# Performance work log

Measured on AMD Instinct MI355X. Metric: run time of the kernel, lower is better.

Reference implementation:

```python
import jax, jax.numpy as jnp
import numpy as np

# Static config (Phi-3-medium style)
HIDDEN = 5120
N_HEADS = 40
N_KV_HEADS = 10
HEAD_DIM = 128  # padded == original here
ROPE_THETA = 10000.0
B, S = 8, 1024  # 8 packed sequences of length 1024 -> T = 8192
T = B * S


def apply_rope(x, pos, theta=ROPE_THETA):
    # x: [T, N, H], pos: [T]  (neox-style split-half rotary over full head dim)
    H = x.shape[-1]
    half = H // 2
    inv_freq = 1.0 / (theta ** (jnp.arange(half, dtype=jnp.float32) * 2.0 / H))
    ang = pos.astype(jnp.float32)[:, None] * inv_freq  # [T, half]
    cos = jnp.cos(ang)[:, None, :]  # [T, 1, half]
    sin = jnp.sin(ang)[:, None, :]
    x1, x2 = x[..., :half], x[..., half:]
    return jnp.concatenate([x1 * cos - x2 * sin, x2 * cos + x1 * sin], axis=-1).astype(x.dtype)


def setup_inputs() -> dict:
    key = jax.random.key(0)
    k1, k2, k3 = jax.random.split(key, 3)
    x = jax.random.normal(k1, (T, HIDDEN), dtype=jnp.float32)
    w_qkv = jax.random.normal(k2, (HIDDEN, N_HEADS + 2 * N_KV_HEADS, HEAD_DIM), dtype=jnp.float32) * (HIDDEN ** -0.5)
    w_o = jax.random.normal(k3, (N_HEADS, HEAD_DIM, HIDDEN), dtype=jnp.float32) * ((N_HEADS * HEAD_DIM) ** -0.5)
    positions = jnp.tile(jnp.arange(S, dtype=jnp.int32), B)  # per-sequence positions
    return {"x": x, "w_qkv": w_qkv, "w_o": w_o, "positions": positions}


def reference(x, w_qkv, w_o, positions):
    # Fused QKV projection: [T, D] x [D, N_total, H] -> [T, N_total, H]
    qkv = jnp.einsum('td,dnh->tnh', x, w_qkv)
    q, k, v = jnp.split(qkv, [N_HEADS, N_HEADS + N_KV_HEADS], axis=1)
    q = apply_rope(q, positions)
    k = apply_rope(k, positions)

    # KV cache is simply the (rope'd) k/v written at token slots (no quantization).
    G = N_HEADS // N_KV_HEADS  # GQA group size
    qb = q.reshape(B, S, N_KV_HEADS, G, HEAD_DIM)
    kb = k.reshape(B, S, N_KV_HEADS, HEAD_DIM)
    vb = v.reshape(B, S, N_KV_HEADS, HEAD_DIM)

    scale = HEAD_DIM ** -0.5
    scores = jnp.einsum('bqkgh,bskh->bkgqs', qb, kb) * scale  # [B,K,G,S,S]
    causal = jnp.tril(jnp.ones((S, S), dtype=bool))
    scores = jnp.where(causal, scores, jnp.finfo(scores.dtype).min)
    probs = jax.nn.softmax(scores, axis=-1)
    out = jnp.einsum('bkgqs,bskh->bqkgh', probs, vb)  # [B,S,K,G,H]
    out = out.reshape(T, N_HEADS, HEAD_DIM)

    o = jnp.einsum('tnh,nhd->td', out, w_o)
    return o
```

## Files before the change

### kernel.cpp

```cpp
#include <hip/hip_runtime.h>
#include <hip/hip_bf16.h>

typedef unsigned short u16;
typedef __attribute__((ext_vector_type(8))) __bf16 bf16x8;
typedef __attribute__((ext_vector_type(4))) float f32x4;

#define GLDS16(gsrc, ldst)                                                         \
  __builtin_amdgcn_global_load_lds(                                               \
      (__attribute__((address_space(1))) const void*)(gsrc),                      \
      (__attribute__((address_space(3))) void*)(ldst), 16, 0, 0)

__device__ __forceinline__ float bf2f(u16 u) {
  union { unsigned int i; float f; } v; v.i = ((unsigned int)u) << 16; return v.f;
}
__device__ __forceinline__ u16 f2bf(float f) {
  union { float f; unsigned int i; } v; v.f = f;
  return (u16)((v.i + 0x7fffu + ((v.i >> 16) & 1u)) >> 16);
}

__global__ void cvt_x_kernel(const float4* __restrict__ in, ushort4* __restrict__ out) {
  size_t i = (size_t)blockIdx.x * 256 + threadIdx.x;
  float4 v = in[i];
  ushort4 o;
  o.x = f2bf(v.x); o.y = f2bf(v.y); o.z = f2bf(v.z); o.w = f2bf(v.w);
  out[i] = o;
}

__global__ void tconv_kernel(const float* __restrict__ in, u16* __restrict__ out,
                             int R, int C) {
  __shared__ float tile[64][65];
  const int c0 = blockIdx.x * 64, r0 = blockIdx.y * 64;
  const int tx = threadIdx.x & 63, ty = threadIdx.x >> 6;
#pragma unroll
  for (int p = 0; p < 16; ++p) {
    int row = p * 4 + ty;
    tile[row][tx] = in[(size_t)(r0 + row) * C + c0 + tx];
  }
  __syncthreads();
#pragma unroll
  for (int p = 0; p < 16; ++p) {
    int row = p * 4 + ty;
    out[(size_t)(c0 + row) * R + r0 + tx] = f2bf(tile[tx][row]);
  }
}

__global__ __launch_bounds__(256, 2) void gemm_bt_kernel(
    const u16* __restrict__ A, const u16* __restrict__ BT,
    float* __restrict__ Cf, u16* __restrict__ Cb, int M, int N, int K,
    int nbx, int nby) {
  const int PW = 8;
  const int per_panel = nby * PW;
  const int bid = blockIdx.x;
  const int panel = bid / per_panel;
  const int rem = bid - panel * per_panel;
  const int pw = min(PW, nbx - panel * PW);
  const int bn = panel * PW + rem % pw;
  const int bm = rem / pw;

  __shared__ __align__(16) u16 As[128 * 32];
  __shared__ __align__(16) u16 Bs[128 * 32];
  const int tid = threadIdx.x;
  const int wave = tid >> 6, lane = tid & 63;
  const int quad = lane >> 4, l16 = lane & 15;
  const int m0 = bm * 128, n0 = bn * 128;
  const int wm = (wave >> 1) * 64, wn = (wave & 1) * 64;
  const int rck = lane >> 2;
  const int kc = (lane & 3) * 8;

  f32x4 acc[4][4] = {};

  const size_t a0 = (size_t)(m0 + 16 * wave + rck) * K;
  const size_t a1 = (size_t)(m0 + 16 * (wave + 4) + rck) * K;
  const size_t b0 = (size_t)(n0 + 16 * wave + rck) * K;
  const size_t b1 = (size_t)(n0 + 16 * (wave + 4) + rck) * K;

  for (int k0 = 0; k0 < K; k0 += 32) {
    __syncthreads();
    GLDS16(A + a0 + k0 + kc, As + 512 * wave);
    GLDS16(A + a1 + k0 + kc, As + 512 * (wave + 4));
    GLDS16(BT + b0 + k0 + kc, Bs + 512 * wave);
    GLDS16(BT + b1 + k0 + kc, Bs + 512 * (wave + 4));
    __syncthreads();
    bf16x8 af[4], bfr[4];
#pragma unroll
    for (int t = 0; t < 4; ++t)
      af[t] = *(const bf16x8*)(As + (wm + 16 * t + l16) * 32 + quad * 8);
#pragma unroll
    for (int t = 0; t < 4; ++t)
      bfr[t] = *(const bf16x8*)(Bs + (wn + 16 * t + l16) * 32 + quad * 8);
#pragma unroll
    for (int mt = 0; mt < 4; ++mt)
#pragma unroll
      for (int nt = 0; nt < 4; ++nt)
        acc[mt][nt] = __builtin_amdgcn_mfma_f32_16x16x32_bf16(af[mt], bfr[nt], acc[mt][nt], 0, 0, 0);
  }
#pragma unroll
  for (int mt = 0; mt < 4; ++mt)
#pragma unroll
    for (int nt = 0; nt < 4; ++nt)
#pragma unroll
      for (int r = 0; r < 4; ++r) {
        int row = m0 + wm + 16 * mt + quad * 4 + r;
        int col = n0 + wn + 16 * nt + l16;
        float v = acc[mt][nt][r];
        if (Cb) Cb[(size_t)row * N + col] = f2bf(v);
        else    Cf[(size_t)row * N + col] = v;
      }
}

__global__ void rope_kernel(u16* __restrict__ qkv, const int* __restrict__ positions) {
  int idx = blockIdx.x * 256 + threadIdx.x;
  int j = idx & 63, t = idx >> 6;
  float inv = exp2f(-(float)j * 0.20762050593046014f);
  float ang = (float)positions[t] * inv;
  float sn, cs;
  sincosf(ang, &sn, &cs);
  u16* row = qkv + (size_t)t * 7680;
#pragma unroll 2
  for (int h = 0; h < 50; ++h) {
    u16* p1 = row + h * 128 + j;
    float x1 = bf2f(p1[0]), x2 = bf2f(p1[64]);
    p1[0] = f2bf(x1 * cs - x2 * sn);
    p1[64] = f2bf(x2 * cs + x1 * sn);
  }
}

__global__ void vtrans_kernel(const u16* __restrict__ qkv, u16* __restrict__ vt) {
  __shared__ u16 tile[64][132];
  const int s0 = blockIdx.x * 64, kvh = blockIdx.y, b = blockIdx.z;
  const int tid = threadIdx.x;
#pragma unroll
  for (int p = 0; p < 8; ++p) {
    int sl = p * 8 + (tid >> 5);
    int d = (tid & 31) * 4;
    const u16* src = qkv + (size_t)(b * 1024 + s0 + sl) * 7680 + (50 + kvh) * 128 + d;
    ushort4 v = *(const ushort4*)src;
    tile[sl][d] = v.x; tile[sl][d + 1] = v.y; tile[sl][d + 2] = v.z; tile[sl][d + 3] = v.w;
  }
  __syncthreads();
#pragma unroll
  for (int p = 0; p < 8; ++p) {
    int d = p * 16 + (tid >> 4);
    int sl = (tid & 15) * 4;
    ushort4 v;
    v.x = tile[sl][d]; v.y = tile[sl + 1][d]; v.z = tile[sl + 2][d]; v.w = tile[sl + 3][d];
    u16* dst = vt + ((size_t)((b * 10 + kvh) * 128) + d) * 1024 + s0 + sl;
    *(ushort4*)dst = v;
  }
}

__global__ __launch_bounds__(256, 2) void attn_kernel(
    const u16* __restrict__ qkv, const u16* __restrict__ vt, u16* __restrict__ ao) {
  __shared__ __align__(16) u16 Ks[4][2048];
  __shared__ __align__(16) u16 VTs[2][4096];
  __shared__ __align__(16) u16 Ps[4][2][1024];

  const int tid = threadIdx.x, wave = tid >> 6, lane = tid & 63;
  const int quad = lane >> 4, l16 = lane & 15;
  const int q0 = blockIdx.x * 128, h = blockIdx.y, b = blockIdx.z;
  const int kvh = h >> 2;
  const float SCALE = 0.08838834764831845f;

  bf16x8 qf[2][4];
#pragma unroll
  for (int mt = 0; mt < 2; ++mt) {
    int t = b * 1024 + q0 + wave * 32 + mt * 16 + l16;
    const u16* qrow = qkv + (size_t)t * 7680 + h * 128;
#pragma unroll
    for (int ks = 0; ks < 4; ++ks)
      qf[mt][ks] = *(const bf16x8*)(qrow + ks * 32 + quad * 8);
  }

  f32x4 oa[2][8] = {};
  float mstate[2][4], lstate[2][4];
#pragma unroll
  for (int mt = 0; mt < 2; ++mt)
#pragma unroll
    for (int r = 0; r < 4; ++r) { mstate[mt][r] = -1e30f; lstate[mt][r] = 0.f; }

  const u16* Kbase = qkv + (size_t)(b * 1024) * 7680 + (40 + kvh) * 128;
  const u16* VTbase = vt + (size_t)((b * 10 + kvh) * 128) * 1024;

  const int nsteps = q0 / 64 + 2;
  for (int step = 0; step < nsteps; ++step) {
    const int s0 = step * 64;
    __syncthreads();
#pragma unroll
    for (int j = 0; j < 4; ++j) {
      int c = 4 * wave + j;
      int ksub = c >> 2, rg = c & 3;
      GLDS16(Kbase + (size_t)(s0 + rg * 16 + (lane >> 2)) * 7680 + ksub * 32 + (lane & 3) * 8,
             &Ks[ksub][rg * 512]);
      int vsub = c >> 3, dg = c & 7;
      GLDS16(VTbase + (size_t)(dg * 16 + (lane >> 2)) * 1024 + s0 + vsub * 32 + (lane & 3) * 8,
             &VTs[vsub][dg * 512]);
    }
    __syncthreads();

    f32x4 sa[2][4] = {};
#pragma unroll
    for (int ks = 0; ks < 4; ++ks) {
      bf16x8 kb[4];
#pragma unroll
      for (int nt = 0; nt < 4; ++nt)
        kb[nt] = *(const bf16x8*)&Ks[ks][(nt * 16 + l16) * 32 + quad * 8];
#pragma unroll
      for (int mt = 0; mt < 2; ++mt)
#pragma unroll
        for (int nt = 0; nt < 4; ++nt)
          sa[mt][nt] = __builtin_amdgcn_mfma_f32_16x16x32_bf16(qf[mt][ks], kb[nt], sa[mt][nt], 0, 0, 0);
    }

#pragma unroll
    for (int mt = 0; mt < 2; ++mt) {
#pragma unroll
      for (int r = 0; r < 4; ++r) {
        int qg = q0 + wave * 32 + mt * 16 + quad * 4 + r;
        float pv[4];
        float rowmax = -1e30f;
#pragma unroll
        for (int nt = 0; nt < 4; ++nt) {
          int sg = s0 + nt * 16 + l16;
          float v = sa[mt][nt][r] * SCALE;
          if (sg > qg) v = -1e30f;
          pv[nt] = v;
          rowmax = fmaxf(rowmax, v);
        }
#pragma unroll
        for (int off = 1; off < 16; off <<= 1)
          rowmax = fmaxf(rowmax, __shfl_xor(rowmax, off));
        float mnew = fmaxf(mstate[mt][r], rowmax);
        float alpha = __expf(mstate[mt][r] - mnew);
        mstate[mt][r] = mnew;
        float rs = 0.f;
#pragma unroll
        for (int nt = 0; nt < 4; ++nt) {
          float p = __expf(pv[nt] - mnew);
          rs += p;
          Ps[wave][nt >> 1][(mt * 16 + quad * 4 + r) * 32 + (nt & 1) * 16 + l16] = f2bf(p);
        }
#pragma unroll
        for (int off = 1; off < 16; off <<= 1)
          rs += __shfl_xor(rs, off);
        lstate[mt][r] = lstate[mt][r] * alpha + rs;
#pragma unroll
        for (int ntd = 0; ntd < 8; ++ntd) oa[mt][ntd][r] *= alpha;
      }
    }
    __syncthreads();

#pragma unroll
    for (int ks2 = 0; ks2 < 2; ++ks2) {
      bf16x8 pf[2];
#pragma unroll
      for (int mt = 0; mt < 2; ++mt)
        pf[mt] = *(const bf16x8*)&Ps[wave][ks2][(mt * 16 + l16) * 32 + quad * 8];
#pragma unroll
      for (int ntd = 0; ntd < 8; ++ntd) {
        bf16x8 vf = *(const bf16x8*)&VTs[ks2][(ntd * 16 + l16) * 32 + quad * 8];
#pragma unroll
        for (int mt = 0; mt < 2; ++mt)
          oa[mt][ntd] = __builtin_amdgcn_mfma_f32_16x16x32_bf16(pf[mt], vf, oa[mt][ntd], 0, 0, 0);
      }
    }
  }

#pragma unroll
  for (int mt = 0; mt < 2; ++mt)
#pragma unroll
    for (int ntd = 0; ntd < 8; ++ntd)
#pragma unroll
      for (int r = 0; r < 4; ++r) {
        int t = b * 1024 + q0 + wave * 32 + mt * 16 + quad * 4 + r;
        int d = ntd * 16 + l16;
        float v = oa[mt][ntd][r] / lstate[mt][r];
        ao[((size_t)t * 40 + h) * 128 + d] = f2bf(v);
      }
}

extern "C" void kernel_launch(void* const* d_in, const int* in_sizes, int n_in,
                              void* d_out, int out_size, void* d_ws, size_t ws_size,
                              hipStream_t stream) {
  const float* x = (const float*)d_in[0];
  const float* wqkv = (const float*)d_in[1];
  const float* wo = (const float*)d_in[2];
  const int* pos = (const int*)d_in[3];
  float* out = (float*)d_out;

  char* ws = (char*)d_ws;
  u16* xb = (u16*)(ws);
  u16* wT = (u16*)(ws + 83886080);
  u16* qkvb = (u16*)(ws + 83886080 + 78643200);
  u16* vt = (u16*)(ws + 83886080 + 78643200 + 125829120);

  cvt_x_kernel<<<40960, 256, 0, stream>>>((const float4*)x, (ushort4*)xb);
  tconv_kernel<<<dim3(120, 80), 256, 0, stream>>>(wqkv, wT, 5120, 7680);
  gemm_bt_kernel<<<60 * 64, 256, 0, stream>>>(xb, wT, nullptr, qkvb, 8192, 7680, 5120, 60, 64);
  rope_kernel<<<2048, 256, 0, stream>>>(qkvb, pos);
  vtrans_kernel<<<dim3(16, 10, 8), 256, 0, stream>>>(qkvb, vt);
  tconv_kernel<<<dim3(80, 80), 256, 0, stream>>>(wo, wT, 5120, 5120);
  attn_kernel<<<dim3(8, 40, 8), 256, 0, stream>>>(qkvb, vt, xb);
  gemm_bt_kernel<<<40 * 64, 256, 0, stream>>>(xb, wT, out, nullptr, 8192, 5120, 5120, 40, 64);
}
```

Measured before the change: 2.333 ms.

## Replace 128x128 GEMM with double-buffered 256x256 tile GEMM using swizzled LDS

Both projection GEMMs now use a 512-thread kernel that computes 256x256 output tiles with 128-wide K steps. Global-to-LDS loads are double-buffered and interleaved with MFMA phases under manual waitcnt and barrier control. The LDS layout is XOR-swizzled to avoid bank conflicts, and the workgroup order is remapped for L2 locality. This targets low data reuse and exposed load latency in the old 128x128 single-buffered loop, at the cost of more LDS and registers per block and reduced occupancy.

```diff
diff --git a/kernel.cpp b/kernel.cpp
--- a/kernel.cpp
+++ b/kernel.cpp
@@ -9,6 +9,23 @@
   __builtin_amdgcn_global_load_lds(                                               \
       (__attribute__((address_space(1))) const void*)(gsrc),                      \
       (__attribute__((address_space(3))) void*)(ldst), 16, 0, 0)
+
+#define BAR() asm volatile("s_barrier" ::: "memory")
+#define LG0()                                            \
+  {                                                      \
+    asm volatile("s_waitcnt lgkmcnt(0)" ::: "memory");   \
+    __builtin_amdgcn_sched_barrier(0);                   \
+  }
+#define VMW2()                                           \
+  {                                                      \
+    asm volatile("s_waitcnt vmcnt(2)" ::: "memory");     \
+    __builtin_amdgcn_sched_barrier(0);                   \
+  }
+#define VMW0()                                           \
+  {                                                      \
+    asm volatile("s_waitcnt vmcnt(0)" ::: "memory");     \
+    __builtin_amdgcn_sched_barrier(0);                   \
+  }
 
 __device__ __forceinline__ float bf2f(u16 u) {
   union { unsigned int i; float f; } v; v.i = ((unsigned int)u) << 16; return v.f;
@@ -44,64 +61,157 @@
   }
 }
 
-__global__ __launch_bounds__(256, 2) void gemm_bt_kernel(
+__device__ __forceinline__ void lda4(bf16x8 a[4][2], const u16* b0, const u16* b1) {
+#pragma unroll
+  for (int mt = 0; mt < 4; ++mt) {
+    a[mt][0] = *(const bf16x8*)(b0 + mt * 1024);
+    a[mt][1] = *(const bf16x8*)(b1 + mt * 1024);
+  }
+}
+__device__ __forceinline__ void ldb2(bf16x8 b[2][2], const u16* b0, const u16* b1) {
+#pragma unroll
+  for (int nt = 0; nt < 2; ++nt) {
+    b[nt][0] = *(const bf16x8*)(b0 + nt * 1024);
+    b[nt][1] = *(const bf16x8*)(b1 + nt * 1024);
+  }
+}
+template <int MH, int NH>
+__device__ __forceinline__ void mma8(f32x4 acc[8][4], const bf16x8 a[4][2], const bf16x8 b[2][2]) {
+  __builtin_amdgcn_s_setprio(1);
+#pragma unroll
+  for (int mt = 0; mt < 4; ++mt)
+#pragma unroll
+    for (int nt = 0; nt < 2; ++nt) {
+      f32x4 c = acc[MH * 4 + mt][NH * 2 + nt];
+      c = __builtin_amdgcn_mfma_f32_16x16x32_bf16(a[mt][0], b[nt][0], c, 0, 0, 0);
+      c = __builtin_amdgcn_mfma_f32_16x16x32_bf16(a[mt][1], b[nt][1], c, 0, 0, 0);
+      acc[MH * 4 + mt][NH * 2 + nt] = c;
+    }
+  __builtin_amdgcn_s_setprio(0);
+}
+
+__global__ __launch_bounds__(512, 2) void gemm_bt256_kernel(
     const u16* __restrict__ A, const u16* __restrict__ BT,
     float* __restrict__ Cf, u16* __restrict__ Cb, int M, int N, int K,
-    int nbx, int nby) {
-  const int PW = 8;
-  const int per_panel = nby * PW;
-  const int bid = blockIdx.x;
-  const int panel = bid / per_panel;
-  const int rem = bid - panel * per_panel;
-  const int pw = min(PW, nbx - panel * PW);
+    int nbm, int nbn) {
+  __shared__ __align__(16) u16 As_[2][16384];
+  __shared__ __align__(16) u16 Bs_[2][16384];
+  u16* As0 = &As_[0][0]; u16* As1 = &As_[1][0];
+  u16* Bs0 = &Bs_[0][0]; u16* Bs1 = &Bs_[1][0];
+
+  const int nwg = nbm * nbn;
+  int wg = (int)blockIdx.x;
+  wg = (wg & 7) * (nwg >> 3) + (wg >> 3);
+  const int PW = 10;
+  const int per_panel = PW * nbm;
+  const int panel = wg / per_panel;
+  const int rem = wg - panel * per_panel;
+  const int pw = min(PW, nbn - panel * PW);
   const int bn = panel * PW + rem % pw;
   const int bm = rem / pw;
-
-  __shared__ __align__(16) u16 As[128 * 32];
-  __shared__ __align__(16) u16 Bs[128 * 32];
+  const int m0 = bm * 256, n0 = bn * 256;
+
   const int tid = threadIdx.x;
   const int wave = tid >> 6, lane = tid & 63;
   const int quad = lane >> 4, l16 = lane & 15;
-  const int m0 = bm * 128, n0 = bn * 128;
-  const int wm = (wave >> 1) * 64, wn = (wave & 1) * 64;
-  const int rck = lane >> 2;
-  const int kc = (lane & 3) * 8;
-
-  f32x4 acc[4][4] = {};
-
-  const size_t a0 = (size_t)(m0 + 16 * wave + rck) * K;
-  const size_t a1 = (size_t)(m0 + 16 * (wave + 4) + rck) * K;
-  const size_t b0 = (size_t)(n0 + 16 * wave + rck) * K;
-  const size_t b1 = (size_t)(n0 + 16 * (wave + 4) + rck) * K;
-
-  for (int k0 = 0; k0 < K; k0 += 32) {
-    __syncthreads();
-    GLDS16(A + a0 + k0 + kc, As + 512 * wave);
-    GLDS16(A + a1 + k0 + kc, As + 512 * (wave + 4));
-    GLDS16(BT + b0 + k0 + kc, Bs + 512 * wave);
-    GLDS16(BT + b1 + k0 + kc, Bs + 512 * (wave + 4));
-    __syncthreads();
-    bf16x8 af[4], bfr[4];
-#pragma unroll
-    for (int t = 0; t < 4; ++t)
-      af[t] = *(const bf16x8*)(As + (wm + 16 * t + l16) * 32 + quad * 8);
-#pragma unroll
-    for (int t = 0; t < 4; ++t)
-      bfr[t] = *(const bf16x8*)(Bs + (wn + 16 * t + l16) * 32 + quad * 8);
-#pragma unroll
-    for (int mt = 0; mt < 4; ++mt)
-#pragma unroll
-      for (int nt = 0; nt < 4; ++nt)
-        acc[mt][nt] = __builtin_amdgcn_mfma_f32_16x16x32_bf16(af[mt], bfr[nt], acc[mt][nt], 0, 0, 0);
-  }
-#pragma unroll
-  for (int mt = 0; mt < 4; ++mt)
+  const int wm = wave >> 2, wn = wave & 3;
+
+  const int rl = lane >> 3;
+  const int cs = ((lane & 7) ^ rl) * 8;
+  const u16* pA = A + (size_t)(m0 + wave * 8 + rl) * K + cs;
+  const u16* pB = BT + (size_t)(n0 + wave * 8 + rl) * K + cs;
+  const size_t r64 = (size_t)64 * K, r128 = (size_t)128 * K;
+
+#define STG(p, hofs, kt, lds)                                         \
+  {                                                                   \
+    GLDS16((p) + (hofs) + (size_t)(kt) * 64, (lds) + wave * 512);     \
+    GLDS16((p) + (hofs) + r64 + (size_t)(kt) * 64, (lds) + 4096 + wave * 512); \
+  }
+
+  const int eo = l16 & 7;
+  const int aoff0 = l16 * 64 + ((quad ^ eo) * 8);
+  const int aoff1 = l16 * 64 + (((4 | quad) ^ eo) * 8);
+  const u16* Ab0 = As0 + wm * 8192;
+  const u16* Ab1 = As1 + wm * 8192;
+  const u16* Bb0 = Bs0 + wn * 4096;
+  const u16* Bb1 = Bs1 + wn * 4096;
+
+  f32x4 acc[8][4] = {};
+  bf16x8 a[4][2], b[2][2];
+
+  const int NIT = K >> 7;
+
+  STG(pA, 0, 0, As0);
+  STG(pA, r128, 0, As0 + 8192);
+  STG(pB, 0, 0, Bs0);
+  STG(pB, r128, 0, Bs0 + 8192);
+  STG(pA, 0, 1, As1);
+  VMW2();
+  BAR();
+
+#pragma unroll 1
+  for (int it = 0; it < NIT; ++it) {
+    const int t = 2 * it;
+    const bool sg = (it < NIT - 1);
+
+    lda4(a, Ab0 + aoff0, Ab0 + aoff1);
+    ldb2(b, Bb0 + aoff0, Bb0 + aoff1);
+    STG(pA, r128, t + 1, As1 + 8192);
+    BAR(); LG0();
+    mma8<0, 0>(acc, a, b);
+    BAR();
+    ldb2(b, Bb0 + 2048 + aoff0, Bb0 + 2048 + aoff1);
+    STG(pB, 0, t + 1, Bs1);
+    BAR(); LG0();
+    mma8<0, 1>(acc, a, b);
+    BAR();
+    lda4(a, Ab0 + 4096 + aoff0, Ab0 + 4096 + aoff1);
+    STG(pB, r128, t + 1, Bs1 + 8192);
+    BAR(); LG0();
+    mma8<1, 1>(acc, a, b);
+    BAR();
+    ldb2(b, Bb0 + aoff0, Bb0 + aoff1);
+    if (sg) STG(pA, 0, t + 2, As0);
+    BAR(); LG0();
+    mma8<1, 0>(acc, a, b);
+    if (sg) { VMW2(); } else { VMW0(); }
+    BAR();
+
+    lda4(a, Ab1 + aoff0, Ab1 + aoff1);
+    ldb2(b, Bb1 + aoff0, Bb1 + aoff1);
+    if (sg) STG(pA, r128, t + 2, As0 + 8192);
+    BAR(); LG0();
+    mma8<0, 0>(acc, a, b);
+    BAR();
+    ldb2(b, Bb1 + 2048 + aoff0, Bb1 + 2048 + aoff1);
+    if (sg) STG(pB, 0, t + 2, Bs0);
+    BAR(); LG0();
+    mma8<0, 1>(acc, a, b);
+    BAR();
+    lda4(a, Ab1 + 4096 + aoff0, Ab1 + 4096 + aoff1);
+    if (sg) STG(pB, r128, t + 2, Bs0 + 8192);
+    BAR(); LG0();
+    mma8<1, 1>(acc, a, b);
+    BAR();
+    ldb2(b, Bb1 + aoff0, Bb1 + aoff1);
+    if (sg) STG(pA, 0, t + 3, As1);
+    BAR(); LG0();
+    mma8<1, 0>(acc, a, b);
+    if (sg) { VMW2(); } else { VMW0(); }
+    BAR();
+  }
+#undef STG
+
+  const int crow0 = m0 + wm * 128 + quad * 4;
+  const int ccol0 = n0 + wn * 64 + l16;
+#pragma unroll
+  for (int mt = 0; mt < 8; ++mt)
 #pragma unroll
     for (int nt = 0; nt < 4; ++nt)
 #pragma unroll
       for (int r = 0; r < 4; ++r) {
-        int row = m0 + wm + 16 * mt + quad * 4 + r;
-        int col = n0 + wn + 16 * nt + l16;
+        int row = crow0 + mt * 16 + r;
+        int col = ccol0 + nt * 16;
         float v = acc[mt][nt][r];
         if (Cb) Cb[(size_t)row * N + col] = f2bf(v);
         else    Cf[(size_t)row * N + col] = v;
@@ -295,10 +405,10 @@
 
   cvt_x_kernel<<<40960, 256, 0, stream>>>((const float4*)x, (ushort4*)xb);
   tconv_kernel<<<dim3(120, 80), 256, 0, stream>>>(wqkv, wT, 5120, 7680);
-  gemm_bt_kernel<<<60 * 64, 256, 0, stream>>>(xb, wT, nullptr, qkvb, 8192, 7680, 5120, 60, 64);
+  gemm_bt256_kernel<<<32 * 30, 512, 0, stream>>>(xb, wT, nullptr, qkvb, 8192, 7680, 5120, 32, 30);
   rope_kernel<<<2048, 256, 0, stream>>>(qkvb, pos);
   vtrans_kernel<<<dim3(16, 10, 8), 256, 0, stream>>>(qkvb, vt);
   tconv_kernel<<<dim3(80, 80), 256, 0, stream>>>(wo, wT, 5120, 5120);
   attn_kernel<<<dim3(8, 40, 8), 256, 0, stream>>>(qkvb, vt, xb);
-  gemm_bt_kernel<<<40 * 64, 256, 0, stream>>>(xb, wT, out, nullptr, 8192, 5120, 5120, 40, 64);
-}
+  gemm_bt256_kernel<<<32 * 20, 512, 0, stream>>>(xb, wT, out, nullptr, 8192, 5120, 5120, 32, 20);
+}
```

Result: faster. 1.967 ms (-15.7%).
